# Performance work log

Measured on AMD Instinct MI355X. Metric: run time of the kernel, lower is better.

## Reference

```python
import jax, jax.numpy as jnp
import numpy as np

EMBED_DIM = 1024
NUM_HEADS = 16
HEAD_DIM = EMBED_DIM // NUM_HEADS
SPARSITY_LAMBDA = 0.01
B, S = 2, 2048


def setup_inputs() -> dict:
    key = jax.random.key(0)
    ks = jax.random.split(key, 10)
    scale = 0.02
    inp = {
        "x": jax.random.normal(ks[0], (B, S, EMBED_DIM), dtype=jnp.float32),
        "Wq": jax.random.normal(ks[1], (EMBED_DIM, EMBED_DIM), dtype=jnp.float32) * scale,
        "bq": jnp.zeros((EMBED_DIM,), dtype=jnp.float32),
        "Wk": jax.random.normal(ks[2], (EMBED_DIM, EMBED_DIM), dtype=jnp.float32) * scale,
        "bk": jnp.zeros((EMBED_DIM,), dtype=jnp.float32),
        "Wv": jax.random.normal(ks[3], (EMBED_DIM, EMBED_DIM), dtype=jnp.float32) * scale,
        "bv": jnp.zeros((EMBED_DIM,), dtype=jnp.float32),
        "Wo": jax.random.normal(ks[4], (EMBED_DIM, EMBED_DIM), dtype=jnp.float32) * scale,
        "bo": jnp.zeros((EMBED_DIM,), dtype=jnp.float32),
        "z": jax.random.normal(ks[5], (NUM_HEADS,), dtype=jnp.float32),
    }
    return inp


def reference(x, Wq, bq, Wk, bk, Wv, bv, Wo, bo, z):
    # Linear layers (torch Linear: y = x @ W.T + b); W here stored as [out, in]
    def split_heads(t):  # [B,S,E] -> [B,H,S,D]
        return t.reshape(B, S, NUM_HEADS, HEAD_DIM).transpose(0, 2, 1, 3)

    q = split_heads(x @ Wq.T + bq)
    k = split_heads(x @ Wk.T + bk)
    v = split_heads(x @ Wv.T + bv)

    scores = jnp.einsum("bhsd,bhtd->bhst", q, k) / jnp.sqrt(jnp.float32(HEAD_DIM))
    gate = jax.nn.sigmoid(z)  # [H], per-head scalar gate on raw scores
    scores = scores * gate[None, :, None, None]
    probs = jax.nn.softmax(scores, axis=-1)
    ctx = jnp.einsum("bhst,bhtd->bhsd", probs, v)  # [B,H,S,D]
    ctx = ctx.transpose(0, 2, 1, 3).reshape(B, S, EMBED_DIM)
    out = ctx @ Wo.T + bo
    penalty = jnp.sum(jax.nn.sigmoid(z)) * SPARSITY_LAMBDA
    return out, penalty
```

## Files before the change

### kernel.cpp

```cpp
#include <hip/hip_runtime.h>

typedef unsigned short ushort_t;
typedef __bf16 bf16x8 __attribute__((ext_vector_type(8)));
typedef ushort_t u16x8 __attribute__((ext_vector_type(8)));
typedef float f32x4 __attribute__((ext_vector_type(4)));

#define DEVI __device__ __forceinline__

constexpr int Ed = 1024;
constexpr int Hh = 16;
constexpr int Dd = 64;
constexpr int Ss = 2048;
constexpr int Mm = 4096;

constexpr int NX4 = Mm * Ed / 4;
constexpr int NW4 = Ed * Ed / 4;

DEVI ushort_t f2bf(float f) {
    union { float f; unsigned int i; } v; v.f = f;
    unsigned int r = v.i + 0x7fffu + ((v.i >> 16) & 1u);
    return (ushort_t)(r >> 16);
}
DEVI ushort_t f2bf_hi(float f) {
    union { float f; unsigned int i; } v; v.f = f;
    return (ushort_t)(v.i >> 16);
}
DEVI float fast_exp2(float x) {
    float r;
    asm("v_exp_f32 %0, %1" : "=v"(r) : "v"(x));
    return r;
}

__global__ __launch_bounds__(256) void cvt_all(
    const float* __restrict__ x,  const float* __restrict__ Wq,
    const float* __restrict__ Wk, const float* __restrict__ Wv,
    const float* __restrict__ Wo,
    ushort_t* __restrict__ xb,  ushort_t* __restrict__ Wqb,
    ushort_t* __restrict__ Wkb, ushort_t* __restrict__ Wvb,
    ushort_t* __restrict__ Wob)
{
    int i = blockIdx.x * 256 + threadIdx.x;
    const float* s; ushort_t* d; int off;
    if (i < NX4)                { s = x;  d = xb;  off = i; }
    else if (i < NX4 + NW4)     { s = Wq; d = Wqb; off = i - NX4; }
    else if (i < NX4 + 2 * NW4) { s = Wk; d = Wkb; off = i - NX4 - NW4; }
    else if (i < NX4 + 3 * NW4) { s = Wv; d = Wvb; off = i - NX4 - 2 * NW4; }
    else                        { s = Wo; d = Wob; off = i - NX4 - 3 * NW4; }
    float4 v = ((const float4*)s)[off];
    ushort4 o; o.x = f2bf(v.x); o.y = f2bf(v.y); o.z = f2bf(v.z); o.w = f2bf(v.w);
    ((ushort4*)d)[off] = o;
}

DEVI void gld16(const void* g, void* l) {
    __builtin_amdgcn_global_load_lds(
        (__attribute__((address_space(1))) void*)(g),
        (__attribute__((address_space(3))) void*)(l), 16, 0, 0);
}

DEVI void gemm_core(const ushort_t* __restrict__ A, const ushort_t* __restrict__ W,
                    ushort_t* As, ushort_t* Bs, int tm, int tn, int K,
                    f32x4 acc[4][4])
{
    const int tid  = threadIdx.x;
    const int w    = tid >> 6;
    const int lane = tid & 63;
    const int quad = lane >> 4;
    const int l15  = lane & 15;
    const int wy   = w >> 1, wx = w & 1;
    const int rowc = lane >> 3;
    const int col8s = (((lane & 7) ^ rowc) * 8);
    const int swq  = l15 & 7;

    for (int k0 = 0; k0 < K; k0 += 64) {
        __syncthreads();
#pragma unroll
        for (int i = 0; i < 4; ++i) {
            int chunk = w * 4 + i;
            int row = chunk * 8 + rowc;
            gld16(A + (size_t)(tm + row) * K + k0 + col8s, (char*)As + chunk * 1024);
            gld16(W + (size_t)(tn + row) * K + k0 + col8s, (char*)Bs + chunk * 1024);
        }
        __syncthreads();
#pragma unroll
        for (int ks = 0; ks < 64; ks += 32) {
            const int k4 = ks >> 3;
            bf16x8 a[4], b[4];
#pragma unroll
            for (int mi = 0; mi < 4; ++mi)
                a[mi] = *(const bf16x8*)&As[(wy * 64 + mi * 16 + l15) * 64
                                            + (((quad + k4) ^ swq) * 8)];
#pragma unroll
            for (int ni = 0; ni < 4; ++ni)
                b[ni] = *(const bf16x8*)&Bs[(wx * 64 + ni * 16 + l15) * 64
                                            + (((quad + k4) ^ swq) * 8)];
#pragma unroll
            for (int mi = 0; mi < 4; ++mi)
#pragma unroll
                for (int ni = 0; ni < 4; ++ni)
                    acc[mi][ni] = __builtin_amdgcn_mfma_f32_16x16x32_bf16(
                        a[mi], b[ni], acc[mi][ni], 0, 0, 0);
        }
    }
}

__global__ __launch_bounds__(256, 3) void qkv_gemm(
    const ushort_t* __restrict__ x,
    const ushort_t* __restrict__ Wq, const float* __restrict__ bq,
    const ushort_t* __restrict__ Wk, const float* __restrict__ bk,
    const ushort_t* __restrict__ Wv, const float* __restrict__ bv,
    ushort_t* __restrict__ qo, ushort_t* __restrict__ ko, ushort_t* __restrict__ vto)
{
    __shared__ __align__(16) ushort_t As[128 * 64];
    __shared__ __align__(16) ushort_t Bs[128 * 64];
    const ushort_t* W; const float* bias; ushort_t* outp; int vmode;
    if (blockIdx.z == 0)      { W = Wq; bias = bq; outp = qo;  vmode = 0; }
    else if (blockIdx.z == 1) { W = Wk; bias = bk; outp = ko;  vmode = 0; }
    else                      { W = Wv; bias = bv; outp = vto; vmode = 1; }

    const int tm = blockIdx.x * 128, tn = blockIdx.y * 128;
    f32x4 acc[4][4] = {};
    gemm_core(x, W, As, Bs, tm, tn, Ed, acc);

    const int tid = threadIdx.x, w = tid >> 6, lane = tid & 63;
    const int quad = lane >> 4, l15 = lane & 15;
    const int wy = w >> 1, wx = w & 1;
#pragma unroll
    for (int ni = 0; ni < 4; ++ni) {
        int gc = tn + wx * 64 + ni * 16 + l15;
        float bb = bias[gc];
        int h = gc >> 6, d = gc & 63;
#pragma unroll
        for (int mi = 0; mi < 4; ++mi) {
#pragma unroll
            for (int r = 0; r < 4; ++r) {
                int gr = tm + wy * 64 + mi * 16 + quad * 4 + r;
                int b_ = gr >> 11, s_ = gr & 2047;
                float v = acc[mi][ni][r] + bb;
                size_t addr;
                if (vmode == 0) addr = ((size_t)(b_ * Hh + h) * Ss + s_) * Dd + d;
                else            addr = ((size_t)(b_ * Hh + h) * Dd + d) * Ss + s_;
                outp[addr] = f2bf_hi(v);
            }
        }
    }
}

__global__ __launch_bounds__(256, 3) void out_gemm(
    const ushort_t* __restrict__ ctx, const ushort_t* __restrict__ Wo,
    const float* __restrict__ bo, const float* __restrict__ z,
    float* __restrict__ out)
{
    __shared__ __align__(16) ushort_t As[128 * 64];
    __shared__ __align__(16) ushort_t Bs[64 * 64];
    const int tm = blockIdx.x * 128, tn = blockIdx.y * 64;

    const int tid  = threadIdx.x;
    const int w    = tid >> 6;
    const int lane = tid & 63;
    const int quad = lane >> 4;
    const int l15  = lane & 15;
    const int wy   = w >> 1, wx = w & 1;
    const int rowc = lane >> 3;
    const int col8s = (((lane & 7) ^ rowc) * 8);
    const int swq  = l15 & 7;

    f32x4 acc[4][2] = {};
    for (int k0 = 0; k0 < Ed; k0 += 64) {
        __syncthreads();
#pragma unroll
        for (int i = 0; i < 4; ++i) {
            int chunk = w * 4 + i;
            int row = chunk * 8 + rowc;
            gld16(ctx + (size_t)(tm + row) * Ed + k0 + col8s, (char*)As + chunk * 1024);
        }
#pragma unroll
        for (int i = 0; i < 2; ++i) {
            int chunk = w * 2 + i;
            int row = chunk * 8 + rowc;
            gld16(Wo + (size_t)(tn + row) * Ed + k0 + col8s, (char*)Bs + chunk * 1024);
        }
        __syncthreads();
#pragma unroll
        for (int ks = 0; ks < 64; ks += 32) {
            const int k4 = ks >> 3;
            bf16x8 a[4], b[2];
#pragma unroll
            for (int mi = 0; mi < 4; ++mi)
                a[mi] = *(const bf16x8*)&As[(wy * 64 + mi * 16 + l15) * 64
                                            + (((quad + k4) ^ swq) * 8)];
#pragma unroll
            for (int ni = 0; ni < 2; ++ni)
                b[ni] = *(const bf16x8*)&Bs[(wx * 32 + ni * 16 + l15) * 64
                                            + (((quad + k4) ^ swq) * 8)];
#pragma unroll
            for (int mi = 0; mi < 4; ++mi)
#pragma unroll
                for (int ni = 0; ni < 2; ++ni)
                    acc[mi][ni] = __builtin_amdgcn_mfma_f32_16x16x32_bf16(
                        a[mi], b[ni], acc[mi][ni], 0, 0, 0);
        }
    }

#pragma unroll
    for (int ni = 0; ni < 2; ++ni) {
        int gc = tn + wx * 32 + ni * 16 + l15;
        float bb = bo[gc];
#pragma unroll
        for (int mi = 0; mi < 4; ++mi)
#pragma unroll
            for (int r = 0; r < 4; ++r) {
                int gr = tm + wy * 64 + mi * 16 + quad * 4 + r;
                out[(size_t)gr * Ed + gc] = acc[mi][ni][r] + bb;
            }
    }

    if (blockIdx.x == 0 && blockIdx.y == 0 && tid == 0) {
        float s = 0.f;
        for (int hh = 0; hh < Hh; ++hh) s += 1.f / (1.f + __expf(-z[hh]));
        out[(size_t)Mm * Ed] = s * 0.01f;
    }
}

__global__ __launch_bounds__(256, 2) void attn(
    const ushort_t* __restrict__ Q, const ushort_t* __restrict__ Kk,
    const ushort_t* __restrict__ Vt, const float* __restrict__ z,
    ushort_t* __restrict__ ctx)
{
    __shared__ __align__(16) ushort_t Ks[2][64 * 64];
    __shared__ __align__(16) ushort_t Ps[4][32 * 68];

    const int tid = threadIdx.x, w = tid >> 6, lane = tid & 63;
    const int quad = lane >> 4, l15 = lane & 15;
    const int lin = blockIdx.x + 16 * blockIdx.y;
    const int qt = lin >> 5;
    const int bh = (lin & 7) * 4 + ((lin >> 3) & 3);
    const int h = bh & (Hh - 1), b_ = bh >> 4;
    const size_t base = (size_t)bh * Ss * Dd;

    const float gate = 1.f / (1.f + __expf(-z[h]));
    const float scl2 = gate * 0.125f * 1.44269504f;

    bf16x8 aQ[2][2];
#pragma unroll
    for (int m = 0; m < 2; ++m)
#pragma unroll
        for (int c = 0; c < 2; ++c)
            aQ[m][c] = *(const bf16x8*)&Q[base
                + (size_t)(qt * 128 + w * 32 + m * 16 + l15) * Dd + c * 32 + quad * 8];

    const int rowA = w * 16 + (lane >> 3);
    const int rowB = rowA + 8;
    const int gsA  = (lane & 7) ^ (rowA & 7);
    const int gsB  = (lane & 7) ^ (rowB & 7);
    const ushort_t* kSrcA = Kk + base + (size_t)rowA * Dd + gsA * 8;
    const ushort_t* kSrcB = Kk + base + (size_t)rowB * Dd + gsB * 8;
    const ushort_t* vBase = Vt + base + (size_t)l15 * Ss + quad * 8;

    f32x4 accO[2][4] = {};
    float lsum[2][4] = {};

    const int swq = (l15 & 7) * 8;

    gld16(kSrcA, &Ks[0][(w * 2) * 512]);
    gld16(kSrcB, &Ks[0][(w * 2 + 1) * 512]);

    for (int kt = 0; kt < Ss / 64; ++kt) {
        const int cur = kt & 1, nxt = cur ^ 1;
        __syncthreads();

        bf16x8 vf[2][4];
#pragma unroll
        for (int ni = 0; ni < 4; ++ni) {
            const ushort_t* vp = vBase + (size_t)(ni * 16) * Ss + kt * 64;
            vf[0][ni] = *(const bf16x8*)(vp);
            vf[1][ni] = *(const bf16x8*)(vp + 32);
        }

        if (kt + 1 < Ss / 64) {
            gld16(kSrcA + (size_t)(kt + 1) * 64 * Dd, &Ks[nxt][(w * 2) * 512]);
            gld16(kSrcB + (size_t)(kt + 1) * 64 * Dd, &Ks[nxt][(w * 2 + 1) * 512]);
        }

        f32x4 sAcc[2][4] = {};
#pragma unroll
        for (int ni = 0; ni < 4; ++ni) {
            bf16x8 b0 = *(const bf16x8*)&Ks[cur][(ni * 16 + l15) * 64 + ((quad * 8) ^ swq)];
            bf16x8 b1 = *(const bf16x8*)&Ks[cur][(ni * 16 + l15) * 64 + (((quad + 4) * 8) ^ swq)];
#pragma unroll
            for (int m = 0; m < 2; ++m) {
                sAcc[m][ni] = __builtin_amdgcn_mfma_f32_16x16x32_bf16(aQ[m][0], b0, sAcc[m][ni], 0, 0, 0);
                sAcc[m][ni] = __builtin_amdgcn_mfma_f32_16x16x32_bf16(aQ[m][1], b1, sAcc[m][ni], 0, 0, 0);
            }
        }

#pragma unroll
        for (int m = 0; m < 2; ++m)
#pragma unroll
            for (int ni = 0; ni < 4; ++ni)
#pragma unroll
                for (int r = 0; r < 4; ++r) {
                    float p = fast_exp2(sAcc[m][ni][r] * scl2);
                    lsum[m][r] += p;
                    Ps[w][(m * 16 + quad * 4 + r) * 68 + ni * 16 + l15] = f2bf_hi(p);
                }

#pragma unroll
        for (int c = 0; c < 2; ++c) {
            bf16x8 aP0 = *(const bf16x8*)&Ps[w][l15 * 68 + c * 32 + quad * 8];
            bf16x8 aP1 = *(const bf16x8*)&Ps[w][(16 + l15) * 68 + c * 32 + quad * 8];
#pragma unroll
            for (int ni = 0; ni < 4; ++ni) {
                accO[0][ni] = __builtin_amdgcn_mfma_f32_16x16x32_bf16(aP0, vf[c][ni], accO[0][ni], 0, 0, 0);
                accO[1][ni] = __builtin_amdgcn_mfma_f32_16x16x32_bf16(aP1, vf[c][ni], accO[1][ni], 0, 0, 0);
            }
        }
    }

#pragma unroll
    for (int m = 0; m < 2; ++m)
#pragma unroll
        for (int r = 0; r < 4; ++r) {
            lsum[m][r] += __shfl_xor(lsum[m][r], 1);
            lsum[m][r] += __shfl_xor(lsum[m][r], 2);
            lsum[m][r] += __shfl_xor(lsum[m][r], 4);
            lsum[m][r] += __shfl_xor(lsum[m][r], 8);
        }

#pragma unroll
    for (int m = 0; m < 2; ++m)
#pragma unroll
        for (int r = 0; r < 4; ++r) {
            int srow = qt * 128 + w * 32 + m * 16 + quad * 4 + r;
            float inv = 1.f / lsum[m][r];
#pragma unroll
            for (int ni = 0; ni < 4; ++ni) {
                int d = ni * 16 + l15;
                ctx[((size_t)(b_ * Ss + srow)) * Ed + h * Dd + d] = f2bf_hi(accO[m][ni][r] * inv);
            }
        }
}

extern "C" void kernel_launch(void* const* d_in, const int* in_sizes, int n_in,
                              void* d_out, int out_size, void* d_ws, size_t ws_size,
                              hipStream_t stream) {
    const float* x  = (const float*)d_in[0];
    const float* Wq = (const float*)d_in[1];
    const float* bq = (const float*)d_in[2];
    const float* Wk = (const float*)d_in[3];
    const float* bk = (const float*)d_in[4];
    const float* Wv = (const float*)d_in[5];
    const float* bv = (const float*)d_in[6];
    const float* Wo = (const float*)d_in[7];
    const float* bo = (const float*)d_in[8];
    const float* z  = (const float*)d_in[9];
    float* out = (float*)d_out;

    ushort_t* xb  = (ushort_t*)d_ws;
    ushort_t* Wqb = xb  + (size_t)Mm * Ed;
    ushort_t* Wkb = Wqb + (size_t)Ed * Ed;
    ushort_t* Wvb = Wkb + (size_t)Ed * Ed;
    ushort_t* Wob = Wvb + (size_t)Ed * Ed;
    ushort_t* qw  = Wob + (size_t)Ed * Ed;
    ushort_t* kw  = qw + (size_t)Mm * Ed;
    ushort_t* vT  = kw + (size_t)Mm * Ed;
    ushort_t* cx  = vT + (size_t)Mm * Ed;

    dim3 blk(256);
    cvt_all<<<dim3((NX4 + 4 * NW4) / 256), blk, 0, stream>>>(
        x, Wq, Wk, Wv, Wo, xb, Wqb, Wkb, Wvb, Wob);
    qkv_gemm<<<dim3(Mm / 128, Ed / 128, 3), blk, 0, stream>>>(
        xb, Wqb, bq, Wkb, bk, Wvb, bv, qw, kw, vT);
    attn<<<dim3(Ss / 128, 2 * Hh), blk, 0, stream>>>(qw, kw, vT, z, cx);
    out_gemm<<<dim3(Mm / 128, Ed / 64), blk, 0, stream>>>(cx, Wob, bo, z, out);
}
```

Baseline: 227.5 us.

## Double K tile to 128 keys, add MFMA priority hints, pack V-transpose stores

The attention kernel now stages 128 keys of K per double-buffered shared-memory tile and processes them in two 64-key sub-steps. This halves the number of block barriers and prefetch issues per key. MFMA sections are wrapped in s_setprio so matrix work from different waves interleaves better. The QKV projection epilogue for V now packs four bf16 values into one 8-byte store instead of four scalar 2-byte stores. The extra shared memory (32 KB for K) may reduce occupancy at 2 blocks per CU.

```diff
diff --git a/kernel.cpp b/kernel.cpp
--- a/kernel.cpp
+++ b/kernel.cpp
@@ -4,6 +4,7 @@
 typedef __bf16 bf16x8 __attribute__((ext_vector_type(8)));
 typedef ushort_t u16x8 __attribute__((ext_vector_type(8)));
 typedef float f32x4 __attribute__((ext_vector_type(4)));
+typedef unsigned int u32x2 __attribute__((ext_vector_type(2)));
 
 #define DEVI __device__ __forceinline__
 
@@ -24,6 +25,10 @@
 DEVI ushort_t f2bf_hi(float f) {
     union { float f; unsigned int i; } v; v.f = f;
     return (ushort_t)(v.i >> 16);
+}
+DEVI unsigned int fbits(float f) {
+    union { float f; unsigned int i; } v; v.f = f;
+    return v.i;
 }
 DEVI float fast_exp2(float x) {
     float r;
@@ -124,22 +129,41 @@
     const int tid = threadIdx.x, w = tid >> 6, lane = tid & 63;
     const int quad = lane >> 4, l15 = lane & 15;
     const int wy = w >> 1, wx = w & 1;
-#pragma unroll
-    for (int ni = 0; ni < 4; ++ni) {
-        int gc = tn + wx * 64 + ni * 16 + l15;
-        float bb = bias[gc];
-        int h = gc >> 6, d = gc & 63;
-#pragma unroll
-        for (int mi = 0; mi < 4; ++mi) {
-#pragma unroll
-            for (int r = 0; r < 4; ++r) {
-                int gr = tm + wy * 64 + mi * 16 + quad * 4 + r;
-                int b_ = gr >> 11, s_ = gr & 2047;
-                float v = acc[mi][ni][r] + bb;
-                size_t addr;
-                if (vmode == 0) addr = ((size_t)(b_ * Hh + h) * Ss + s_) * Dd + d;
-                else            addr = ((size_t)(b_ * Hh + h) * Dd + d) * Ss + s_;
-                outp[addr] = f2bf_hi(v);
+    if (vmode == 0) {
+#pragma unroll
+        for (int ni = 0; ni < 4; ++ni) {
+            int gc = tn + wx * 64 + ni * 16 + l15;
+            float bb = bias[gc];
+            int h = gc >> 6, d = gc & 63;
+#pragma unroll
+            for (int mi = 0; mi < 4; ++mi) {
+#pragma unroll
+                for (int r = 0; r < 4; ++r) {
+                    int gr = tm + wy * 64 + mi * 16 + quad * 4 + r;
+                    int b_ = gr >> 11, s_ = gr & 2047;
+                    float v = acc[mi][ni][r] + bb;
+                    outp[((size_t)(b_ * Hh + h) * Ss + s_) * Dd + d] = f2bf_hi(v);
+                }
+            }
+        }
+    } else {
+#pragma unroll
+        for (int ni = 0; ni < 4; ++ni) {
+            int gc = tn + wx * 64 + ni * 16 + l15;
+            float bb = bias[gc];
+            int h = gc >> 6, d = gc & 63;
+#pragma unroll
+            for (int mi = 0; mi < 4; ++mi) {
+                int gr0 = tm + wy * 64 + mi * 16 + quad * 4;
+                int b_ = gr0 >> 11, s0 = gr0 & 2047;
+                unsigned int u0 = fbits(acc[mi][ni][0] + bb);
+                unsigned int u1 = fbits(acc[mi][ni][1] + bb);
+                unsigned int u2 = fbits(acc[mi][ni][2] + bb);
+                unsigned int u3 = fbits(acc[mi][ni][3] + bb);
+                u32x2 pk;
+                pk[0] = (u1 & 0xffff0000u) | (u0 >> 16);
+                pk[1] = (u3 & 0xffff0000u) | (u2 >> 16);
+                *(u32x2*)&outp[((size_t)(b_ * Hh + h) * Dd + d) * Ss + s0] = pk;
             }
         }
     }
@@ -226,7 +250,7 @@
     const ushort_t* __restrict__ Vt, const float* __restrict__ z,
     ushort_t* __restrict__ ctx)
 {
-    __shared__ __align__(16) ushort_t Ks[2][64 * 64];
+    __shared__ __align__(16) ushort_t Ks[2][128 * 64];
     __shared__ __align__(16) ushort_t Ps[4][32 * 68];
 
     const int tid = threadIdx.x, w = tid >> 6, lane = tid & 63;
@@ -248,12 +272,12 @@
             aQ[m][c] = *(const bf16x8*)&Q[base
                 + (size_t)(qt * 128 + w * 32 + m * 16 + l15) * Dd + c * 32 + quad * 8];
 
-    const int rowA = w * 16 + (lane >> 3);
-    const int rowB = rowA + 8;
-    const int gsA  = (lane & 7) ^ (rowA & 7);
-    const int gsB  = (lane & 7) ^ (rowB & 7);
-    const ushort_t* kSrcA = Kk + base + (size_t)rowA * Dd + gsA * 8;
-    const ushort_t* kSrcB = Kk + base + (size_t)rowB * Dd + gsB * 8;
+    const int rowc = lane >> 3;
+    const int gs   = ((lane & 7) ^ rowc) * 8;
+    const ushort_t* kSrc[4];
+#pragma unroll
+    for (int i = 0; i < 4; ++i)
+        kSrc[i] = Kk + base + (size_t)(w * 32 + i * 8 + rowc) * Dd + gs;
     const ushort_t* vBase = Vt + base + (size_t)l15 * Ss + quad * 8;
 
     f32x4 accO[2][4] = {};
@@ -261,58 +285,68 @@
 
     const int swq = (l15 & 7) * 8;
 
-    gld16(kSrcA, &Ks[0][(w * 2) * 512]);
-    gld16(kSrcB, &Ks[0][(w * 2 + 1) * 512]);
-
-    for (int kt = 0; kt < Ss / 64; ++kt) {
+#pragma unroll
+    for (int i = 0; i < 4; ++i)
+        gld16(kSrc[i], (char*)Ks[0] + (w * 4 + i) * 1024);
+
+    for (int kt = 0; kt < Ss / 128; ++kt) {
         const int cur = kt & 1, nxt = cur ^ 1;
         __syncthreads();
 
-        bf16x8 vf[2][4];
-#pragma unroll
-        for (int ni = 0; ni < 4; ++ni) {
-            const ushort_t* vp = vBase + (size_t)(ni * 16) * Ss + kt * 64;
-            vf[0][ni] = *(const bf16x8*)(vp);
-            vf[1][ni] = *(const bf16x8*)(vp + 32);
-        }
-
-        if (kt + 1 < Ss / 64) {
-            gld16(kSrcA + (size_t)(kt + 1) * 64 * Dd, &Ks[nxt][(w * 2) * 512]);
-            gld16(kSrcB + (size_t)(kt + 1) * 64 * Dd, &Ks[nxt][(w * 2 + 1) * 512]);
-        }
-
-        f32x4 sAcc[2][4] = {};
-#pragma unroll
-        for (int ni = 0; ni < 4; ++ni) {
-            bf16x8 b0 = *(const bf16x8*)&Ks[cur][(ni * 16 + l15) * 64 + ((quad * 8) ^ swq)];
-            bf16x8 b1 = *(const bf16x8*)&Ks[cur][(ni * 16 + l15) * 64 + (((quad + 4) * 8) ^ swq)];
-#pragma unroll
-            for (int m = 0; m < 2; ++m) {
-                sAcc[m][ni] = __builtin_amdgcn_mfma_f32_16x16x32_bf16(aQ[m][0], b0, sAcc[m][ni], 0, 0, 0);
-                sAcc[m][ni] = __builtin_amdgcn_mfma_f32_16x16x32_bf16(aQ[m][1], b1, sAcc[m][ni], 0, 0, 0);
-            }
-        }
-
-#pragma unroll
-        for (int m = 0; m < 2; ++m)
-#pragma unroll
-            for (int ni = 0; ni < 4; ++ni)
-#pragma unroll
-                for (int r = 0; r < 4; ++r) {
-                    float p = fast_exp2(sAcc[m][ni][r] * scl2);
-                    lsum[m][r] += p;
-                    Ps[w][(m * 16 + quad * 4 + r) * 68 + ni * 16 + l15] = f2bf_hi(p);
+        if (kt + 1 < Ss / 128) {
+#pragma unroll
+            for (int i = 0; i < 4; ++i)
+                gld16(kSrc[i] + (size_t)(kt + 1) * 128 * Dd,
+                      (char*)Ks[nxt] + (w * 4 + i) * 1024);
+        }
+
+#pragma unroll
+        for (int sub = 0; sub < 2; ++sub) {
+            bf16x8 vf[2][4];
+#pragma unroll
+            for (int ni = 0; ni < 4; ++ni) {
+                const ushort_t* vp = vBase + (size_t)(ni * 16) * Ss + kt * 128 + sub * 64;
+                vf[0][ni] = *(const bf16x8*)(vp);
+                vf[1][ni] = *(const bf16x8*)(vp + 32);
+            }
+
+            f32x4 sAcc[2][4] = {};
+            __builtin_amdgcn_s_setprio(1);
+#pragma unroll
+            for (int ni = 0; ni < 4; ++ni) {
+                bf16x8 b0 = *(const bf16x8*)&Ks[cur][(sub * 64 + ni * 16 + l15) * 64 + ((quad * 8) ^ swq)];
+                bf16x8 b1 = *(const bf16x8*)&Ks[cur][(sub * 64 + ni * 16 + l15) * 64 + (((quad + 4) * 8) ^ swq)];
+#pragma unroll
+                for (int m = 0; m < 2; ++m) {
+                    sAcc[m][ni] = __builtin_amdgcn_mfma_f32_16x16x32_bf16(aQ[m][0], b0, sAcc[m][ni], 0, 0, 0);
+                    sAcc[m][ni] = __builtin_amdgcn_mfma_f32_16x16x32_bf16(aQ[m][1], b1, sAcc[m][ni], 0, 0, 0);
                 }
-
-#pragma unroll
-        for (int c = 0; c < 2; ++c) {
-            bf16x8 aP0 = *(const bf16x8*)&Ps[w][l15 * 68 + c * 32 + quad * 8];
-            bf16x8 aP1 = *(const bf16x8*)&Ps[w][(16 + l15) * 68 + c * 32 + quad * 8];
-#pragma unroll
-            for (int ni = 0; ni < 4; ++ni) {
-                accO[0][ni] = __builtin_amdgcn_mfma_f32_16x16x32_bf16(aP0, vf[c][ni], accO[0][ni], 0, 0, 0);
-                accO[1][ni] = __builtin_amdgcn_mfma_f32_16x16x32_bf16(aP1, vf[c][ni], accO[1][ni], 0, 0, 0);
-            }
+            }
+            __builtin_amdgcn_s_setprio(0);
+
+#pragma unroll
+            for (int m = 0; m < 2; ++m)
+#pragma unroll
+                for (int ni = 0; ni < 4; ++ni)
+#pragma unroll
+                    for (int r = 0; r < 4; ++r) {
+                        float p = fast_exp2(sAcc[m][ni][r] * scl2);
+                        lsum[m][r] += p;
+                        Ps[w][(m * 16 + quad * 4 + r) * 68 + ni * 16 + l15] = f2bf_hi(p);
+                    }
+
+            __builtin_amdgcn_s_setprio(1);
+#pragma unroll
+            for (int c = 0; c < 2; ++c) {
+                bf16x8 aP0 = *(const bf16x8*)&Ps[w][l15 * 68 + c * 32 + quad * 8];
+                bf16x8 aP1 = *(const bf16x8*)&Ps[w][(16 + l15) * 68 + c * 32 + quad * 8];
+#pragma unroll
+                for (int ni = 0; ni < 4; ++ni) {
+                    accO[0][ni] = __builtin_amdgcn_mfma_f32_16x16x32_bf16(aP0, vf[c][ni], accO[0][ni], 0, 0, 0);
+                    accO[1][ni] = __builtin_amdgcn_mfma_f32_16x16x32_bf16(aP1, vf[c][ni], accO[1][ni], 0, 0, 0);
+                }
+            }
+            __builtin_amdgcn_s_setprio(0);
         }
     }
 
```

New measurement: 209.6 us. 7.9% less time.
